# Kernel tuning notes

Hardware: AMD Instinct MI355X
Metric: run time of the kernel (lower is better)

## Reference

```python
import jax, jax.numpy as jnp
import numpy as np

B, S, D, H, HID = 8, 1024, 768, 12, 3072
HD = D // H
EPS = 1e-5


def layernorm(x, g, b):
    mu = jnp.mean(x, axis=-1, keepdims=True)
    var = jnp.mean(jnp.square(x - mu), axis=-1, keepdims=True)
    return (x - mu) * jax.lax.rsqrt(var + EPS) * g + b


def setup_inputs() -> dict:
    key = jax.random.key(0)
    ks = jax.random.split(key, 8)
    s_d = 1.0 / np.sqrt(D)
    s_h = 1.0 / np.sqrt(HID)
    return {
        "x": jax.random.normal(ks[0], (B, S, D), jnp.float32),
        # attention projections (stored as [in, out])
        "wq": jax.random.normal(ks[1], (D, D), jnp.float32) * s_d,
        "bq": jnp.zeros((D,), jnp.float32),
        "wk": jax.random.normal(ks[2], (D, D), jnp.float32) * s_d,
        "bk": jnp.zeros((D,), jnp.float32),
        "wv": jax.random.normal(ks[3], (D, D), jnp.float32) * s_d,
        "bv": jnp.zeros((D,), jnp.float32),
        # layernorms
        "ln1_g": jnp.ones((D,), jnp.float32),
        "ln1_b": jnp.zeros((D,), jnp.float32),
        "ln2_g": jnp.ones((D,), jnp.float32),
        "ln2_b": jnp.zeros((D,), jnp.float32),
        # MLP
        "w_in": jax.random.normal(ks[4], (D, HID), jnp.float32) * s_d,
        "b_in": jnp.zeros((HID,), jnp.float32),
        "w_out": jax.random.normal(ks[5], (HID, D), jnp.float32) * s_h,
        "b_out": jnp.zeros((D,), jnp.float32),
    }


def reference(x, wq, bq, wk, bk, wv, bv, ln1_g, ln1_b, ln2_g, ln2_b,
              w_in, b_in, w_out, b_out):
    scale = HD ** -0.5
    # --- MHSA (note: original forward never applies out_proj) ---
    q = (x @ wq + bq).reshape(B, S, H, HD).transpose(0, 2, 1, 3)  # [B,H,S,hd]
    k = (x @ wk + bk).reshape(B, S, H, HD).transpose(0, 2, 1, 3)
    v = (x @ wv + bv).reshape(B, S, H, HD).transpose(0, 2, 1, 3)
    scores = jnp.einsum("bhqd,bhkd->bhqk", q, k)  # full NxN, as in source
    attn = jax.nn.softmax(scores * scale, axis=-1)
    ctx = jnp.einsum("bhqk,bhkd->bhqd", attn, v)
    ctx = ctx.transpose(0, 2, 1, 3).reshape(B, S, D)
    # --- residual: pre_ln applied to attention OUTPUT (as in source) ---
    x = x + layernorm(ctx, ln1_g, ln1_b)
    # --- MLP: GELU after BOTH linears (as in source), dropout=0 ---
    h = jax.nn.gelu(layernorm(x, ln2_g, ln2_b) @ w_in + b_in, approximate=False)
    h = jax.nn.gelu(h @ w_out + b_out, approximate=False)
    return x + h
```

## Files before the change

kernel.cpp:

```cpp
#include <hip/hip_runtime.h>
#include <math.h>

typedef __attribute__((ext_vector_type(8))) short short8;
typedef __attribute__((ext_vector_type(4))) short short4v;
typedef __attribute__((ext_vector_type(4))) float f32x4;

#define MFMA16(a, b, c) __builtin_amdgcn_mfma_f32_16x16x32_bf16(a, b, c, 0, 0, 0)

__device__ __forceinline__ short f2bf(float f) {
    union { float f; unsigned u; } v; v.f = f;
    unsigned r = v.u + 0x7fffu + ((v.u >> 16) & 1u);
    return (short)(r >> 16);
}
__device__ __forceinline__ float bf2f(short s) {
    union { unsigned u; float f; } v; v.u = ((unsigned)(unsigned short)s) << 16;
    return v.f;
}
__device__ __forceinline__ float gelu(float v) {
    float u = v * (1.0f + 0.044715f * v * v);
    float e = exp2f(-2.3021184f * u);
    return v * __builtin_amdgcn_rcpf(1.0f + e);
}
__device__ __forceinline__ void async16(const short* g, short* l) {
    __builtin_amdgcn_global_load_lds((const __attribute__((address_space(1))) void*)g,
                                     (__attribute__((address_space(3))) void*)l, 16, 0, 0);
}

__device__ __forceinline__ short8 build_pfrag(int lg, float x0, float x1, float x2, float x3,
                                              float x4, float x5, float x6, float x7) {
    unsigned a0, a1, b0, b1;
    asm("v_cvt_pk_bf16_f32 %0, %1, %2" : "=v"(a0) : "v"(x0), "v"(x1));
    asm("v_cvt_pk_bf16_f32 %0, %1, %2" : "=v"(a1) : "v"(x2), "v"(x3));
    asm("v_cvt_pk_bf16_f32 %0, %1, %2" : "=v"(b0) : "v"(x4), "v"(x5));
    asm("v_cvt_pk_bf16_f32 %0, %1, %2" : "=v"(b1) : "v"(x6), "v"(x7));
    unsigned u0 = (lg < 2) ? b0 : a0, u1 = (lg < 2) ? b1 : a1;
    unsigned v0 = (unsigned)__shfl_xor((int)u0, 32), v1 = (unsigned)__shfl_xor((int)u1, 32);
    unsigned w0 = (lg < 2) ? a0 : b0, w1 = (lg < 2) ? a1 : b1;
    bool sw = ((lg ^ (lg >> 1)) & 1) != 0;
    unsigned s0 = sw ? w0 : v0, s1 = sw ? w1 : v1;
    unsigned r0 = (unsigned)__shfl_xor((int)s0, 16), r1 = (unsigned)__shfl_xor((int)s1, 16);
    union { unsigned u[4]; short8 s; } o;
    o.u[0] = (lg & 1) ? r0 : ((lg == 0) ? w0 : v0);
    o.u[1] = (lg & 1) ? r1 : ((lg == 0) ? w1 : v1);
    o.u[2] = (lg & 1) ? ((lg == 1) ? v0 : w0) : r0;
    o.u[3] = (lg & 1) ? ((lg == 1) ? v1 : w1) : r1;
    return o.s;
}

__global__ __launch_bounds__(256) void cast_kernel(const float* __restrict__ in,
                                                   short* __restrict__ out, int n4) {
    int i = blockIdx.x * 256 + threadIdx.x;
    if (i < n4) {
        float4 v = ((const float4*)in)[i];
        short4v o;
        o.x = f2bf(v.x); o.y = f2bf(v.y); o.z = f2bf(v.z); o.w = f2bf(v.w);
        ((short4v*)out)[i] = o;
    }
}

__global__ __launch_bounds__(256) void concat_bias(const float* __restrict__ a,
                                                   const float* __restrict__ b,
                                                   const float* __restrict__ c,
                                                   float* __restrict__ o) {
    int i = blockIdx.x * 256 + threadIdx.x;
    if (i < 768) o[i] = a[i];
    else if (i < 1536) o[i] = b[i - 768];
    else if (i < 2304) o[i] = c[i - 1536];
}

__global__ __launch_bounds__(256) void transpose_cast(const float* __restrict__ in,
                                                      short* __restrict__ out,
                                                      int K, int N) {
    __shared__ float tile[32][33];
    int n0 = blockIdx.x * 32, k0 = blockIdx.y * 32;
    int tx = threadIdx.x & 31, ty = threadIdx.x >> 5;
#pragma unroll
    for (int r = 0; r < 4; ++r)
        tile[ty + r * 8][tx] = in[(size_t)(k0 + ty + r * 8) * N + n0 + tx];
    __syncthreads();
#pragma unroll
    for (int r = 0; r < 4; ++r) {
        int rr = ty + r * 8;
        out[(size_t)(n0 + rr) * K + k0 + tx] = f2bf(tile[tx][rr]);
    }
}

__global__ __launch_bounds__(256) void transpose_v(const short* __restrict__ in,
                                                   short* __restrict__ out) {
    __shared__ short tile[32][33];
    const int bh = blockIdx.z;
    const int s0 = blockIdx.y * 32, d0 = blockIdx.x * 32;
    const short* src = in + (size_t)bh * 1024 * 64;
    short* dst = out + (size_t)bh * 64 * 1024;
    int tx = threadIdx.x & 31, ty = threadIdx.x >> 5;
#pragma unroll
    for (int r = 0; r < 4; ++r)
        tile[ty + r * 8][tx] = src[(size_t)(s0 + ty + r * 8) * 64 + d0 + tx];
    __syncthreads();
#pragma unroll
    for (int r = 0; r < 4; ++r) {
        int rr = ty + r * 8;
        dst[(size_t)(d0 + rr) * 1024 + s0 + tx] = tile[tx][rr];
    }
}

template <int EPI, int NF>
__global__ __launch_bounds__(256) void gemm_kernel(const short* __restrict__ A,
                                                   const short* __restrict__ Bt,
                                                   const float* __restrict__ bias,
                                                   void* __restrict__ Cout,
                                                   const float* __restrict__ resid,
                                                   int M, int N, int K) {
    const int TN = NF * 32;
    const int t = threadIdx.x;
    const int wid = t >> 6, lane = t & 63;
    const int wm = wid >> 1, wn = wid & 1;
    const int lr = lane & 15, lg = lane >> 4;
    const int row0 = blockIdx.y * 128, col0 = blockIdx.x * TN;

    __shared__ __align__(16) short As[128][32];
    __shared__ __align__(16) short Bs[NF * 32][32];

    f32x4 acc[4][NF];
#pragma unroll
    for (int i = 0; i < 4; ++i)
#pragma unroll
        for (int j = 0; j < NF; ++j) acc[i][j] = (f32x4){0.f, 0.f, 0.f, 0.f};

    const short* Ag = A + (size_t)(row0 + wid * 16 + (lane >> 2)) * K + (lane & 3) * 8;
    const short* Bg = Bt + (size_t)(col0 + wid * 16 + (lane >> 2)) * K + (lane & 3) * 8;

    for (int k0 = 0; k0 < K; k0 += 32) {
        __syncthreads();
        async16(Ag + k0, &As[wid * 16][0]);
        async16(Ag + (size_t)64 * K + k0, &As[64 + wid * 16][0]);
        async16(Bg + k0, &Bs[wid * 16][0]);
        if constexpr (NF == 4)
            async16(Bg + (size_t)64 * K + k0, (short*)Bs + (64 + wid * 16) * 32);
        __syncthreads();

        short8 af[4], bfr[NF];
#pragma unroll
        for (int i = 0; i < 4; ++i)
            af[i] = *(short8*)((short*)As + (wm * 64 + i * 16 + lr) * 32 + lg * 8);
#pragma unroll
        for (int i = 0; i < NF; ++i)
            bfr[i] = *(short8*)((short*)Bs + (wn * (NF * 16) + i * 16 + lr) * 32 + lg * 8);
#pragma unroll
        for (int mi = 0; mi < 4; ++mi)
#pragma unroll
            for (int ni = 0; ni < NF; ++ni)
                acc[mi][ni] = MFMA16(af[mi], bfr[ni], acc[mi][ni]);
    }

#pragma unroll
    for (int mi = 0; mi < 4; ++mi)
#pragma unroll
        for (int ni = 0; ni < NF; ++ni)
#pragma unroll
            for (int r = 0; r < 4; ++r) {
                int row = row0 + wm * 64 + mi * 16 + lg * 4 + r;
                int col = col0 + wn * (NF * 16) + ni * 16 + lr;
                float v = acc[mi][ni][r] + bias[col];
                if constexpr (EPI == 0) {
                    unsigned uc = (unsigned)col;
                    unsigned m = uc / 768u;
                    unsigned rest = uc - m * 768u;
                    unsigned h = rest >> 6, d = rest & 63u;
                    int b = row >> 10, s_ = row & 1023;
                    ((short*)Cout)[((((size_t)m * 96 + (size_t)b * 12 + h) * 1024 + s_) * 64) + d] = f2bf(v);
                } else if constexpr (EPI == 1) {
                    ((short*)Cout)[(size_t)row * N + col] = f2bf(gelu(v));
                } else {
                    size_t idx = (size_t)row * N + col;
                    ((float*)Cout)[idx] = resid[idx] + gelu(v);
                }
            }
}

__global__ __launch_bounds__(256) void attn_kernel(const short* __restrict__ Q,
                                                   const short* __restrict__ Kg,
                                                   const short* __restrict__ VTg,
                                                   short* __restrict__ ctx) {
    const int bh = blockIdx.x;
    const int q0 = blockIdx.y * 64;
    const int t = threadIdx.x, wid = t >> 6, lane = t & 63;
    const int lr = lane & 15, lg = lane >> 4;
    const float C = 0.18033688011f;

    __shared__ __align__(16) short Qs[64][72];
    __shared__ __align__(16) short Ks[64][72];
    __shared__ __align__(16) short Vt[64][72];

    const size_t base = (size_t)bh * 1024 * 64;
    const size_t vbase = (size_t)bh * 64 * 1024;

#pragma unroll
    for (int pass = 0; pass < 2; ++pass) {
        int slot = pass * 256 + t;
        int r = slot >> 3, ds = (slot & 7) << 3;
        *(short8*)&Qs[r][ds] = *(const short8*)(Q + base + (size_t)(q0 + r) * 64 + ds);
    }
    __syncthreads();
    short8 qf[2];
    qf[0] = *(short8*)&Qs[wid * 16 + lr][lg * 8];
    qf[1] = *(short8*)&Qs[wid * 16 + lr][32 + lg * 8];

    f32x4 oacc[4];
#pragma unroll
    for (int i = 0; i < 4; ++i) oacc[i] = (f32x4){0.f, 0.f, 0.f, 0.f};
    float mrun = -1e30f, lrun = 0.f;

    for (int kt = 0; kt < 16; ++kt) {
        __syncthreads();
        const int krow0 = kt * 64;
#pragma unroll
        for (int pass = 0; pass < 2; ++pass) {
            int slot = pass * 256 + t;
            int r = slot >> 3, ds = (slot & 7) << 3;
            *(short8*)&Ks[r][ds] = *(const short8*)(Kg + base + (size_t)(krow0 + r) * 64 + ds);
            *(short8*)&Vt[r][ds] = *(const short8*)(VTg + vbase + (size_t)r * 1024 + krow0 + ds);
        }
        __syncthreads();

        f32x4 sfr[4];
#pragma unroll
        for (int cf = 0; cf < 4; ++cf) {
            f32x4 s = (f32x4){0.f, 0.f, 0.f, 0.f};
            short8 kf0 = *(short8*)&Ks[cf * 16 + lr][lg * 8];
            short8 kf1 = *(short8*)&Ks[cf * 16 + lr][32 + lg * 8];
            s = MFMA16(kf0, qf[0], s);
            s = MFMA16(kf1, qf[1], s);
            sfr[cf] = s;
        }

        float tv[16];
#pragma unroll
        for (int cf = 0; cf < 4; ++cf)
#pragma unroll
            for (int r = 0; r < 4; ++r) tv[cf * 4 + r] = sfr[cf][r] * C;
        float mx = tv[0];
#pragma unroll
        for (int i = 1; i < 16; ++i) mx = fmaxf(mx, tv[i]);
        mx = fmaxf(mx, __shfl_xor(mx, 16));
        mx = fmaxf(mx, __shfl_xor(mx, 32));
        float mnew = fmaxf(mrun, mx);
        float fac = exp2f(mrun - mnew);
        float p[16];
        float rs = 0.f;
#pragma unroll
        for (int i = 0; i < 16; ++i) { p[i] = exp2f(tv[i] - mnew); rs += p[i]; }
        rs += __shfl_xor(rs, 16);
        rs += __shfl_xor(rs, 32);
        lrun = lrun * fac + rs;
        mrun = mnew;

#pragma unroll
        for (int r = 0; r < 4; ++r) {
            float fr = __shfl(fac, lg * 4 + r);
#pragma unroll
            for (int df = 0; df < 4; ++df) oacc[df][r] *= fr;
        }

        short8 pf0 = build_pfrag(lg, p[0], p[1], p[2], p[3], p[4], p[5], p[6], p[7]);
        short8 pf1 = build_pfrag(lg, p[8], p[9], p[10], p[11], p[12], p[13], p[14], p[15]);
#pragma unroll
        for (int df = 0; df < 4; ++df) {
            short8 vf0 = *(short8*)&Vt[df * 16 + lr][lg * 8];
            oacc[df] = MFMA16(pf0, vf0, oacc[df]);
        }
#pragma unroll
        for (int df = 0; df < 4; ++df) {
            short8 vf1 = *(short8*)&Vt[df * 16 + lr][32 + lg * 8];
            oacc[df] = MFMA16(pf1, vf1, oacc[df]);
        }
    }

    const int b = bh / 12, h = bh % 12;
    float rinv[4];
#pragma unroll
    for (int r = 0; r < 4; ++r) {
        float lr_ = __shfl(lrun, lg * 4 + r);
        rinv[r] = __builtin_amdgcn_rcpf(lr_);
    }
#pragma unroll
    for (int df = 0; df < 4; ++df)
#pragma unroll
        for (int r = 0; r < 4; ++r) {
            int q = q0 + wid * 16 + lg * 4 + r;
            int d = df * 16 + lr;
            float o = oacc[df][r] * rinv[r];
            ctx[((size_t)b * 1024 + q) * 768 + h * 64 + d] = f2bf(o);
        }
}

__global__ __launch_bounds__(256) void ln_fused(const float* __restrict__ x,
                                                const short* __restrict__ ctx,
                                                const float* __restrict__ g1,
                                                const float* __restrict__ b1,
                                                const float* __restrict__ g2,
                                                const float* __restrict__ b2,
                                                float* __restrict__ x2,
                                                short* __restrict__ ln2b) {
    const int row = blockIdx.x, t = threadIdx.x;
    const int wid = t >> 6, lane = t & 63;
    __shared__ float red[8];

    float c[3], xv[3];
#pragma unroll
    for (int j = 0; j < 3; ++j) {
        int idx = t + 256 * j;
        c[j] = bf2f(ctx[(size_t)row * 768 + idx]);
        xv[j] = x[(size_t)row * 768 + idx];
    }
    float s = c[0] + c[1] + c[2];
    float s2 = c[0] * c[0] + c[1] * c[1] + c[2] * c[2];
#pragma unroll
    for (int off = 32; off > 0; off >>= 1) { s += __shfl_down(s, off); s2 += __shfl_down(s2, off); }
    if (lane == 0) { red[wid] = s; red[4 + wid] = s2; }
    __syncthreads();
    s = red[0] + red[1] + red[2] + red[3];
    s2 = red[4] + red[5] + red[6] + red[7];
    float mu = s * (1.0f / 768.0f);
    float rstd = rsqrtf(s2 * (1.0f / 768.0f) - mu * mu + 1e-5f);

    float y[3];
#pragma unroll
    for (int j = 0; j < 3; ++j) {
        int idx = t + 256 * j;
        y[j] = xv[j] + (c[j] - mu) * rstd * g1[idx] + b1[idx];
        x2[(size_t)row * 768 + idx] = y[j];
    }
    __syncthreads();
    s = y[0] + y[1] + y[2];
    s2 = y[0] * y[0] + y[1] * y[1] + y[2] * y[2];
#pragma unroll
    for (int off = 32; off > 0; off >>= 1) { s += __shfl_down(s, off); s2 += __shfl_down(s2, off); }
    if (lane == 0) { red[wid] = s; red[4 + wid] = s2; }
    __syncthreads();
    s = red[0] + red[1] + red[2] + red[3];
    s2 = red[4] + red[5] + red[6] + red[7];
    float mu2 = s * (1.0f / 768.0f);
    float rstd2 = rsqrtf(s2 * (1.0f / 768.0f) - mu2 * mu2 + 1e-5f);
#pragma unroll
    for (int j = 0; j < 3; ++j) {
        int idx = t + 256 * j;
        ln2b[(size_t)row * 768 + idx] = f2bf((y[j] - mu2) * rstd2 * g2[idx] + b2[idx]);
    }
}

extern "C" void kernel_launch(void* const* d_in, const int* in_sizes, int n_in,
                              void* d_out, int out_size, void* d_ws, size_t ws_size,
                              hipStream_t stream) {
    const float* x    = (const float*)d_in[0];
    const float* wq   = (const float*)d_in[1];
    const float* bq   = (const float*)d_in[2];
    const float* wk   = (const float*)d_in[3];
    const float* bk   = (const float*)d_in[4];
    const float* wv   = (const float*)d_in[5];
    const float* bv   = (const float*)d_in[6];
    const float* g1   = (const float*)d_in[7];
    const float* b1   = (const float*)d_in[8];
    const float* g2   = (const float*)d_in[9];
    const float* b2   = (const float*)d_in[10];
    const float* w_in = (const float*)d_in[11];
    const float* b_in = (const float*)d_in[12];
    const float* w_out  = (const float*)d_in[13];
    const float* b_out  = (const float*)d_in[14];
    float* out = (float*)d_out;

    char* ws = (char*)d_ws;
    short* xb     = (short*)(ws + 0);
    short* vT     = (short*)(ws + 0);
    short* qb     = (short*)(ws + 12582912);
    short* kb     = (short*)(ws + 25165824);
    short* vb     = (short*)(ws + 37748736);
    short* h1     = (short*)(ws + 0);
    short* ctx    = (short*)(ws + 50331648);
    float* x2     = (float*)(ws + 62914560);
    float* bqkv   = (float*)(ws + 62914560);
    short* ln2b   = (short*)(ws + 88080384);
    short* wqkvT  = (short*)(ws + 100663296);
    short* w_inT  = (short*)(ws + 104202240);
    short* w_outT = (short*)(ws + 108920832);

    cast_kernel<<<6144, 256, 0, stream>>>(x, xb, 1572864);
    concat_bias<<<9, 256, 0, stream>>>(bq, bk, bv, bqkv);
    transpose_cast<<<dim3(24, 24), 256, 0, stream>>>(wq, wqkvT, 768, 768);
    transpose_cast<<<dim3(24, 24), 256, 0, stream>>>(wk, wqkvT + 768 * 768, 768, 768);
    transpose_cast<<<dim3(24, 24), 256, 0, stream>>>(wv, wqkvT + 2 * 768 * 768, 768, 768);
    transpose_cast<<<dim3(96, 24), 256, 0, stream>>>(w_in, w_inT, 768, 3072);
    transpose_cast<<<dim3(24, 96), 256, 0, stream>>>(w_out, w_outT, 3072, 768);

    gemm_kernel<0, 4><<<dim3(18, 64), 256, 0, stream>>>(xb, wqkvT, bqkv, qb, nullptr, 8192, 2304, 768);

    transpose_v<<<dim3(2, 32, 96), 256, 0, stream>>>(vb, vT);

    attn_kernel<<<dim3(96, 16), 256, 0, stream>>>(qb, kb, vT, ctx);

    ln_fused<<<8192, 256, 0, stream>>>(x, ctx, g1, b1, g2, b2, x2, ln2b);

    gemm_kernel<1, 4><<<dim3(24, 64), 256, 0, stream>>>(ln2b, w_inT, b_in, h1, nullptr, 8192, 3072, 768);
    gemm_kernel<2, 2><<<dim3(12, 64), 256, 0, stream>>>(h1, w_outT, b_out, out, x2, 8192, 768, 3072);
}
```

Before: 404.4 us.

## Double GEMM K-tile to 64 with XOR-swizzled LDS and widen out-proj tile

The GEMM kernel now loads a K-depth of 64 per iteration instead of 32, halving the number of barrier pairs per K sweep. The shared-memory tiles use an XOR swizzle on 16-byte chunks so fragment reads avoid bank conflicts. The final MLP projection switches from a 128x64 to a 128x128 tile, giving more reuse per block but only 384 blocks. The cost is doubled LDS per block, which may lower occupancy, and the smaller grid for the last GEMM may underfill the GPU.

```diff
diff --git a/kernel.cpp b/kernel.cpp
--- a/kernel.cpp
+++ b/kernel.cpp
@@ -118,8 +118,8 @@
     const int lr = lane & 15, lg = lane >> 4;
     const int row0 = blockIdx.y * 128, col0 = blockIdx.x * TN;
 
-    __shared__ __align__(16) short As[128][32];
-    __shared__ __align__(16) short Bs[NF * 32][32];
+    __shared__ __align__(16) short As[128 * 64];
+    __shared__ __align__(16) short Bs[NF * 32 * 64];
 
     f32x4 acc[4][NF];
 #pragma unroll
@@ -127,30 +127,40 @@
 #pragma unroll
         for (int j = 0; j < NF; ++j) acc[i][j] = (f32x4){0.f, 0.f, 0.f, 0.f};
 
-    const short* Ag = A + (size_t)(row0 + wid * 16 + (lane >> 2)) * K + (lane & 3) * 8;
-    const short* Bg = Bt + (size_t)(col0 + wid * 16 + (lane >> 2)) * K + (lane & 3) * 8;
-
-    for (int k0 = 0; k0 < K; k0 += 32) {
+    const int aRow = wid * 8 + (lane >> 3);
+    const int aK = ((lane & 7) ^ (lane >> 3)) << 3;
+    const short* Ag = A + (size_t)(row0 + aRow) * K + aK;
+    const short* Bg = Bt + (size_t)(col0 + aRow) * K + aK;
+    short* AsW = As + wid * 8 * 64;
+    short* BsW = Bs + wid * 8 * 64;
+    const int swz = lr & 7;
+
+    for (int k0 = 0; k0 < K; k0 += 64) {
         __syncthreads();
-        async16(Ag + k0, &As[wid * 16][0]);
-        async16(Ag + (size_t)64 * K + k0, &As[64 + wid * 16][0]);
-        async16(Bg + k0, &Bs[wid * 16][0]);
-        if constexpr (NF == 4)
-            async16(Bg + (size_t)64 * K + k0, (short*)Bs + (64 + wid * 16) * 32);
+#pragma unroll
+        for (int j = 0; j < 4; ++j)
+            async16(Ag + (size_t)(j * 32) * K + k0, AsW + j * 32 * 64);
+#pragma unroll
+        for (int j = 0; j < NF; ++j)
+            async16(Bg + (size_t)(j * 32) * K + k0, BsW + j * 32 * 64);
         __syncthreads();
 
-        short8 af[4], bfr[NF];
-#pragma unroll
-        for (int i = 0; i < 4; ++i)
-            af[i] = *(short8*)((short*)As + (wm * 64 + i * 16 + lr) * 32 + lg * 8);
-#pragma unroll
-        for (int i = 0; i < NF; ++i)
-            bfr[i] = *(short8*)((short*)Bs + (wn * (NF * 16) + i * 16 + lr) * 32 + lg * 8);
-#pragma unroll
-        for (int mi = 0; mi < 4; ++mi)
-#pragma unroll
-            for (int ni = 0; ni < NF; ++ni)
-                acc[mi][ni] = MFMA16(af[mi], bfr[ni], acc[mi][ni]);
+#pragma unroll
+        for (int ks = 0; ks < 2; ++ks) {
+            const int rdofs = ((ks * 4 + lg) ^ swz) << 3;
+            short8 af[4], bfr[NF];
+#pragma unroll
+            for (int i = 0; i < 4; ++i)
+                af[i] = *(short8*)(As + (wm * 64 + i * 16 + lr) * 64 + rdofs);
+#pragma unroll
+            for (int i = 0; i < NF; ++i)
+                bfr[i] = *(short8*)(Bs + (wn * (NF * 16) + i * 16 + lr) * 64 + rdofs);
+#pragma unroll
+            for (int mi = 0; mi < 4; ++mi)
+#pragma unroll
+                for (int ni = 0; ni < NF; ++ni)
+                    acc[mi][ni] = MFMA16(af[mi], bfr[ni], acc[mi][ni]);
+        }
     }
 
 #pragma unroll
@@ -401,5 +411,5 @@
     ln_fused<<<8192, 256, 0, stream>>>(x, ctx, g1, b1, g2, b2, x2, ln2b);
 
     gemm_kernel<1, 4><<<dim3(24, 64), 256, 0, stream>>>(ln2b, w_inT, b_in, h1, nullptr, 8192, 3072, 768);
-    gemm_kernel<2, 2><<<dim3(12, 64), 256, 0, stream>>>(h1, w_outT, b_out, out, x2, 8192, 768, 3072);
-}
+    gemm_kernel<2, 4><<<dim3(6, 64), 256, 0, stream>>>(h1, w_outT, b_out, out, x2, 8192, 768, 3072);
+}
```

New measurement: 392.2 us. -3.0%, faster.
